# Kernel tuning notes

Measured on AMD Instinct MI355X. Metric: run time of the kernel, lower is better.

Reference implementation:

```python
import jax, jax.numpy as jnp
import numpy as np

B, C, T, H, W = 32, 384, 16, 14, 14
K, NUM_SAMPLES, SIGMA = 8, 1000, 0.05
C2 = 2 * C  # ScoreNet doubles embed_dim internally


def setup_inputs() -> dict:
    key = jax.random.key(0)
    ks = jax.random.split(key, 12)
    def rn(k, shape, s=0.02):
        return jax.random.normal(k, shape, dtype=jnp.float32) * s
    return {
        "frames": jax.random.normal(ks[0], (B, C, T, H, W), dtype=jnp.float32),
        "noise": jax.random.normal(ks[1], (B, NUM_SAMPLES, T), dtype=jnp.float32),
        "conv_w": rn(ks[2], (C, C, 1, 3, 3)),
        "conv_b": jnp.zeros((C,), jnp.float32),
        "bn_g": jnp.ones((C,), jnp.float32),
        "bn_b": jnp.zeros((C,), jnp.float32),
        "ln_g": jnp.ones((C2,), jnp.float32),
        "ln_b": jnp.zeros((C2,), jnp.float32),
        "lin_w": rn(ks[3], (C2, C2)),
        "lin_b": jnp.zeros((C2,), jnp.float32),
        "w1": rn(ks[4], (C2, C)), "b1": jnp.zeros((C,), jnp.float32),
        "w2": rn(ks[5], (C, C // 2)), "b2": jnp.zeros((C // 2,), jnp.float32),
        "w3": rn(ks[6], (C // 2, 1)), "b3": jnp.zeros((1,), jnp.float32),
    }


def score_net(frames, conv_w, conv_b, bn_g, bn_b, ln_g, ln_b, lin_w, lin_b,
              w1, b1, w2, b2, w3, b3):
    x = jax.lax.stop_gradient(frames)  # ScoreNet detaches its input
    x = jax.lax.conv_general_dilated(
        x, conv_w, window_strides=(1, 2, 2), padding='VALID',
        dimension_numbers=('NCDHW', 'OIDHW', 'NCDHW'))
    x = x + conv_b[None, :, None, None, None]
    # BatchNorm3d in training mode: biased batch stats over (N,T,H,W)
    m = x.mean(axis=(0, 2, 3, 4))
    v = x.var(axis=(0, 2, 3, 4))
    x = (x - m[None, :, None, None, None]) / jnp.sqrt(v + 1e-5)[None, :, None, None, None]
    x = x * bn_g[None, :, None, None, None] + bn_b[None, :, None, None, None]
    # b c t h w -> b t (h w) c
    b, c, t, h, w = x.shape
    x = jnp.transpose(x, (0, 2, 3, 4, 1)).reshape(b, t, h * w, c)
    x = jnp.concatenate([x.mean(axis=2), x.max(axis=2)], axis=-1)  # [B,T,2C]
    # LayerNorm(2C)
    mu = x.mean(-1, keepdims=True)
    var = x.var(-1, keepdims=True)
    x = (x - mu) / jnp.sqrt(var + 1e-5) * ln_g + ln_b
    x = jax.nn.gelu(x @ lin_w + lin_b, approximate=False)
    local_x = x[..., :C2 // 2]
    global_x = jnp.broadcast_to(x[..., C2 // 2:].mean(axis=1, keepdims=True), (b, t, C2 // 2))
    x = jnp.concatenate([local_x, global_x], axis=-1)
    x = jax.nn.gelu(x @ w1 + b1, approximate=False)
    x = jax.nn.gelu(x @ w2 + b2, approximate=False)
    score = (x @ w3 + b3)[..., 0]  # [B,T]
    smin = score.min(axis=-1, keepdims=True)
    smax = score.max(axis=-1, keepdims=True)
    return (score - smin) / (smax - smin + 1e-5)


def perturbed_indicators(score, noise):
    d = score.shape[-1]
    pert = score[:, None, :] + noise * SIGMA  # [B,N,T]
    idx_top = jnp.sort(jax.lax.top_k(pert, K)[1], axis=-1)        # [B,N,K]
    idx_back = jnp.sort(jax.lax.top_k(-pert, d - K)[1], axis=-1)  # [B,N,T-K]
    ind_top = jax.nn.one_hot(idx_top, d, dtype=jnp.float32).mean(axis=1)   # [B,K,T]
    ind_back = jax.nn.one_hot(idx_back, d, dtype=jnp.float32).mean(axis=1)  # [B,T-K,T]
    return ind_top, ind_back


def reference(frames, noise, conv_w, conv_b, bn_g, bn_b, ln_g, ln_b, lin_w, lin_b,
              w1, b1, w2, b2, w3, b3):
    score = score_net(frames, conv_w, conv_b, bn_g, bn_b, ln_g, ln_b, lin_w, lin_b,
                      w1, b1, w2, b2, w3, b3)  # [B,T]
    ind_top, ind_back = perturbed_indicators(score, noise)
    # b c t h w -> b t (h w c)
    flat = jnp.transpose(frames, (0, 2, 3, 4, 1)).reshape(B, T, H * W * C)
    p_top = jnp.einsum('bkd,bdc->bkc', ind_top, flat)
    p_back = jnp.einsum('bkd,bdc->bkc', ind_back, flat)
    frames_topk = jnp.transpose(p_top.reshape(B, K, H, W, C), (0, 4, 1, 2, 3))
    frames_back = jnp.transpose(p_back.reshape(B, T - K, H, W, C), (0, 4, 1, 2, 3))
    sorted_inds = jnp.argsort(score, axis=1)
    return frames_topk, frames_back, sorted_inds
```

## Files before the change

### kernel.cpp

```cpp
#include <hip/hip_runtime.h>
#include <hip/hip_bf16.h>
#include <cstdint>

#define NB 32
#define NC 384
#define NT 16
#define NH 14
#define NW 14
#define HWI 196
#define HOW 6
#define HWO 36
#define C2 768
#define MCONV (NB*NT*HWO)
#define KCONV 3456
#define TOPK 8
#define NSAMP 1000
#define OUT_TOPK_ELEMS (NB*NC*TOPK*HWI)
#define OUT_INDS_OFF   (2*OUT_TOPK_ELEMS)

#define OFF_FHI  0ull
#define OFF_FLO  77070336ull
#define OFF_WHI  154140672ull
#define OFF_WLO  156794880ull
#define OFF_CONV 159449088ull
#define OFF_PART 0ull
#define OFF_BNSC 221184ull
#define OFF_BNSH 222720ull
#define OFF_Y    224256ull
#define OFF_X1   1797120ull
#define OFF_GM   3369984ull
#define OFF_H1   4992000ull
#define OFF_H2   5778432ull
#define OFF_IND  6171648ull

typedef __attribute__((ext_vector_type(4))) float f32x4;
typedef __attribute__((ext_vector_type(8))) short bf16x8;

__device__ __forceinline__ unsigned short f2bf(float f) {
  unsigned u = __float_as_uint(f);
  unsigned r = (u + 0x7FFFu + ((u >> 16) & 1u)) >> 16;
  return (unsigned short)r;
}
__device__ __forceinline__ float bf2f(unsigned short u) {
  return __uint_as_float(((unsigned)u) << 16);
}

__device__ __forceinline__ void gload_lds16(const void* gptr, void* lptr) {
  __builtin_amdgcn_global_load_lds(
      (const __attribute__((address_space(1))) unsigned int*)gptr,
      (__attribute__((address_space(3))) unsigned int*)lptr, 16, 0, 0);
}

__global__ __launch_bounds__(256)
void split_frames(const float* __restrict__ fr,
                  unsigned short* __restrict__ fhi,
                  unsigned short* __restrict__ flo) {
  __shared__ unsigned int tile[64][197];
  int bid = blockIdx.x;
  int cb = bid % 6, bt = bid / 6;
  int b = bt >> 4, t = bt & 15;
  const float* src = fr + (((size_t)b * NC + cb * 64) * NT + t) * HWI;
  for (int i = threadIdx.x; i < 64 * 49; i += 256) {
    int c = i / 49, q = i - c * 49;
    float4 v = *(const float4*)(src + (size_t)c * (NT * HWI) + q * 4);
    float vv[4] = {v.x, v.y, v.z, v.w};
#pragma unroll
    for (int u = 0; u < 4; ++u) {
      unsigned short h = f2bf(vv[u]);
      unsigned short l = f2bf(vv[u] - bf2f(h));
      tile[c][q * 4 + u] = ((unsigned)h << 16) | (unsigned)l;
    }
  }
  __syncthreads();
  size_t obase = ((size_t)bt * HWI) * NC + cb * 64;
  for (int i = threadIdx.x; i < 196 * 8; i += 256) {
    int hw = i >> 3, c8 = i & 7;
    bf16x8 vh, vl;
#pragma unroll
    for (int u = 0; u < 8; ++u) {
      unsigned p = tile[c8 * 8 + u][hw];
      vh[u] = (short)(p >> 16);
      vl[u] = (short)(p & 0xffff);
    }
    size_t o = obase + (size_t)hw * NC + c8 * 8;
    *(bf16x8*)(fhi + o) = vh;
    *(bf16x8*)(flo + o) = vl;
  }
}

__global__ __launch_bounds__(256)
void split_w(const float* __restrict__ cw,
             unsigned short* __restrict__ whi,
             unsigned short* __restrict__ wlo) {
  int idx = blockIdx.x * 256 + threadIdx.x;
  int co = idx / KCONV;
  int rem = idx - co * KCONV;
  int c9 = rem / NC, ci = rem - c9 * NC;
  float v = cw[((size_t)co * NC + ci) * 9 + c9];
  unsigned short h = f2bf(v);
  unsigned short l = f2bf(v - bf2f(h));
  whi[idx] = h; wlo[idx] = l;
}

__global__ __launch_bounds__(256, 2)
void conv_gemm(const unsigned short* __restrict__ fhi,
               const unsigned short* __restrict__ flo,
               const unsigned short* __restrict__ whi,
               const unsigned short* __restrict__ wlo,
               const float* __restrict__ conv_b,
               float* __restrict__ p0,
               float* __restrict__ p1) {
  __shared__ unsigned short sAhi[128 * 32], sAlo[128 * 32];
  __shared__ unsigned short sBhi[128 * 32], sBlo[128 * 32];
  const int tid = threadIdx.x;
  const int lane = tid & 63;
  const int wv = tid >> 6;
  const int bid = blockIdx.x;
  const int bm = bid % 144;
  const int r  = bid / 144;
  const int bn = r % 3;
  const int kz = r / 3;

  int aoff[2], boff[2];
#pragma unroll
  for (int j = 0; j < 2; ++j) {
    int l = (wv * 2 + j) * 64 + lane;
    int row = l >> 2, chunk = l & 3;
    int m = bm * 128 + row;
    int wo = m % 6; int tmp = m / 6;
    int ho = tmp % 6; tmp /= 6;
    aoff[j] = ((tmp * HWI) + (2 * ho) * NW + 2 * wo) * NC + chunk * 8;
    int co = bn * 128 + row;
    boff[j] = co * KCONV + chunk * 8;
  }

  f32x4 acc[4][4];
#pragma unroll
  for (int i = 0; i < 4; ++i)
#pragma unroll
    for (int j = 0; j < 4; ++j) acc[i][j] = (f32x4){0.f, 0.f, 0.f, 0.f};

  const int wrow = (wv >> 1) * 64;
  const int wcol = (wv & 1) * 64;
  const int fr_row = lane & 15;
  const int fr_k = (lane >> 4) * 8;

  int c9 = kz ? 4 : 0;
  int rem = kz ? 6 : 0;
  for (int s = 0; s < 54; ++s) {
    int kh = c9 / 3, kw = c9 - kh * 3;
    int soffA = (kh * NW + kw) * NC + rem * 32;
    int soffB = c9 * NC + rem * 32;
#pragma unroll
    for (int j = 0; j < 2; ++j) {
      char* ldsA  = (char*)sAhi + (wv * 2 + j) * 1024;
      char* ldsAl = (char*)sAlo + (wv * 2 + j) * 1024;
      char* ldsB  = (char*)sBhi + (wv * 2 + j) * 1024;
      char* ldsBl = (char*)sBlo + (wv * 2 + j) * 1024;
      gload_lds16(fhi + aoff[j] + soffA, ldsA);
      gload_lds16(flo + aoff[j] + soffA, ldsAl);
      gload_lds16(whi + boff[j] + soffB, ldsB);
      gload_lds16(wlo + boff[j] + soffB, ldsBl);
    }
    __syncthreads();
    bf16x8 ah[4], al[4], bh[4], bl[4];
#pragma unroll
    for (int m = 0; m < 4; ++m) {
      int rr = wrow + m * 16 + fr_row;
      ah[m] = *(const bf16x8*)&sAhi[rr * 32 + fr_k];
      al[m] = *(const bf16x8*)&sAlo[rr * 32 + fr_k];
    }
#pragma unroll
    for (int n = 0; n < 4; ++n) {
      int rr = wcol + n * 16 + fr_row;
      bh[n] = *(const bf16x8*)&sBhi[rr * 32 + fr_k];
      bl[n] = *(const bf16x8*)&sBlo[rr * 32 + fr_k];
    }
#pragma unroll
    for (int m = 0; m < 4; ++m)
#pragma unroll
      for (int n = 0; n < 4; ++n) {
        acc[m][n] = __builtin_amdgcn_mfma_f32_16x16x32_bf16(ah[m], bh[n], acc[m][n], 0, 0, 0);
        acc[m][n] = __builtin_amdgcn_mfma_f32_16x16x32_bf16(ah[m], bl[n], acc[m][n], 0, 0, 0);
        acc[m][n] = __builtin_amdgcn_mfma_f32_16x16x32_bf16(al[m], bh[n], acc[m][n], 0, 0, 0);
      }
    __syncthreads();
    if (++rem == 12) { rem = 0; ++c9; }
  }

  float* dst = kz ? p1 : p0;
#pragma unroll
  for (int m = 0; m < 4; ++m)
#pragma unroll
    for (int n = 0; n < 4; ++n) {
      int col = bn * 128 + wcol + n * 16 + (lane & 15);
      float cb = kz ? 0.f : conv_b[col];
#pragma unroll
      for (int j = 0; j < 4; ++j) {
        int row = bm * 128 + wrow + m * 16 + (lane >> 4) * 4 + j;
        dst[(size_t)row * NC + col] = acc[m][n][j] + cb;
      }
    }
}

__global__ __launch_bounds__(384)
void bn_part(const float* __restrict__ p0, const float* __restrict__ p1,
             float* __restrict__ part) {
  int c = threadIdx.x;
  int r0 = blockIdx.x * 256;
  float s = 0.f, sq = 0.f;
  for (int r = 0; r < 256; ++r) {
    size_t off = (size_t)(r0 + r) * NC + c;
    float v = p0[off] + p1[off];
    s += v; sq += v * v;
  }
  part[blockIdx.x * 768 + c] = s;
  part[blockIdx.x * 768 + 384 + c] = sq;
}

__global__ __launch_bounds__(384)
void bn_fin(const float* __restrict__ part, const float* __restrict__ bn_g,
            const float* __restrict__ bn_b, float* __restrict__ bnsc,
            float* __restrict__ bnsh) {
  int c = threadIdx.x;
  float s = 0.f, sq = 0.f;
  for (int i = 0; i < 72; ++i) {
    s += part[i * 768 + c];
    sq += part[i * 768 + 384 + c];
  }
  float mean = s / (float)MCONV;
  float var = sq / (float)MCONV - mean * mean;
  float sc = bn_g[c] / sqrtf(var + 1e-5f);
  bnsc[c] = sc;
  bnsh[c] = bn_b[c] - mean * sc;
}

__global__ __launch_bounds__(384)
void pool_ln(const float* __restrict__ p0, const float* __restrict__ p1,
             const float* __restrict__ bnsc,
             const float* __restrict__ bnsh, const float* __restrict__ ln_g,
             const float* __restrict__ ln_b, float* __restrict__ y) {
  __shared__ float r1[384], r2[384], stats[2];
  int bt = blockIdx.x, c = threadIdx.x;
  float sc = bnsc[c], sh = bnsh[c];
  size_t base = (size_t)bt * HWO * NC + c;
  float sum = 0.f, mx = -1e30f;
  for (int hw = 0; hw < HWO; ++hw) {
    size_t off = base + (size_t)hw * NC;
    float v = (p0[off] + p1[off]) * sc + sh;
    sum += v;
    mx = fmaxf(mx, v);
  }
  float meanv = sum * (1.f / 36.f);
  r1[c] = meanv + mx;
  r2[c] = meanv * meanv + mx * mx;
  __syncthreads();
  for (int s = 192; s >= 6; s >>= 1) {
    if (c < s) { r1[c] += r1[c + s]; r2[c] += r2[c + s]; }
    __syncthreads();
  }
  if (c == 0) {
    float S1 = 0.f, S2 = 0.f;
    for (int i = 0; i < 6; ++i) { S1 += r1[i]; S2 += r2[i]; }
    float mu = S1 / (float)C2;
    float var = S2 / (float)C2 - mu * mu;
    stats[0] = mu;
    stats[1] = 1.0f / sqrtf(var + 1e-5f);
  }
  __syncthreads();
  float mu = stats[0], rstd = stats[1];
  y[(size_t)bt * C2 + c] = (meanv - mu) * rstd * ln_g[c] + ln_b[c];
  y[(size_t)bt * C2 + 384 + c] = (mx - mu) * rstd * ln_g[384 + c] + ln_b[384 + c];
}

template <int GELU, int X2>
__global__ __launch_bounds__(256)
void gemm64(const float* __restrict__ A, const float* __restrict__ gmv,
            const float* __restrict__ Wm,
            const float* __restrict__ bias, float* __restrict__ Cm,
            int K, int N) {
  __shared__ float As[64][17];
  __shared__ float Bs[16][68];
  int tid = threadIdx.x;
  int tx = tid & 15, ty = tid >> 4;
  int m0 = blockIdx.y * 64, n0 = blockIdx.x * 64;
  int ar = tid >> 2, ak = (tid & 3) * 4;
  int br = tid >> 4, bc = (tid & 15) * 4;
  float acc[4][4] = {};
  for (int kt = 0; kt < K; kt += 16) {
    int kcol = kt + ak;
    float4 av;
    if (X2 && kcol >= 384)
      av = *(const float4*)(gmv + ((m0 + ar) >> 4) * 384 + (kcol - 384));
    else
      av = *(const float4*)(A + (size_t)(m0 + ar) * K + kcol);
    float4 bv = *(const float4*)(Wm + (size_t)(kt + br) * N + n0 + bc);
    As[ar][ak + 0] = av.x; As[ar][ak + 1] = av.y;
    As[ar][ak + 2] = av.z; As[ar][ak + 3] = av.w;
    Bs[br][bc + 0] = bv.x; Bs[br][bc + 1] = bv.y;
    Bs[br][bc + 2] = bv.z; Bs[br][bc + 3] = bv.w;
    __syncthreads();
#pragma unroll
    for (int kk = 0; kk < 16; ++kk) {
      float a0 = As[ty * 4 + 0][kk], a1 = As[ty * 4 + 1][kk];
      float a2 = As[ty * 4 + 2][kk], a3 = As[ty * 4 + 3][kk];
      float b0 = Bs[kk][tx * 4 + 0], b1 = Bs[kk][tx * 4 + 1];
      float b2 = Bs[kk][tx * 4 + 2], b3 = Bs[kk][tx * 4 + 3];
      acc[0][0] += a0 * b0; acc[0][1] += a0 * b1; acc[0][2] += a0 * b2; acc[0][3] += a0 * b3;
      acc[1][0] += a1 * b0; acc[1][1] += a1 * b1; acc[1][2] += a1 * b2; acc[1][3] += a1 * b3;
      acc[2][0] += a2 * b0; acc[2][1] += a2 * b1; acc[2][2] += a2 * b2; acc[2][3] += a2 * b3;
      acc[3][0] += a3 * b0; acc[3][1] += a3 * b1; acc[3][2] += a3 * b2; acc[3][3] += a3 * b3;
    }
    __syncthreads();
  }
#pragma unroll
  for (int i = 0; i < 4; ++i) {
    int row = m0 + ty * 4 + i;
#pragma unroll
    for (int j = 0; j < 4; ++j) {
      int col = n0 + tx * 4 + j;
      float v = acc[i][j] + bias[col];
      if (GELU) v = 0.5f * v * (1.0f + erff(v * 0.70710678118654752f));
      Cm[(size_t)row * N + col] = v;
    }
  }
}

__global__ __launch_bounds__(384)
void gmean_k(const float* __restrict__ x1, float* __restrict__ gm) {
  int b = blockIdx.x, c = threadIdx.x;
  float s = 0.f;
  for (int t = 0; t < NT; ++t) s += x1[((size_t)b * NT + t) * C2 + 384 + c];
  gm[b * 384 + c] = s * (1.f / 16.f);
}

__global__ __launch_bounds__(256)
void score_head(const float* __restrict__ h2, const float* __restrict__ w3,
                const float* __restrict__ b3, const float* __restrict__ noise,
                float* __restrict__ ind, float* __restrict__ out_inds) {
  int b = blockIdx.x;
  int tid = threadIdx.x;
  int lane = tid & 63, wv = tid >> 6;
  __shared__ float sv[16], sn[16];
  __shared__ unsigned cnt[256];
  for (int t = wv; t < 16; t += 4) {
    const float* hr = h2 + ((size_t)b * 16 + t) * 192;
    float p = 0.f;
    for (int i = lane; i < 192; i += 64) p += hr[i] * w3[i];
#pragma unroll
    for (int off = 32; off; off >>= 1) p += __shfl_down(p, off, 64);
    if (lane == 0) sv[t] = p + b3[0];
  }
  cnt[tid] = 0;
  __syncthreads();
  if (tid == 0) {
    float mn = sv[0], mx = sv[0];
    for (int t = 1; t < 16; ++t) { mn = fminf(mn, sv[t]); mx = fmaxf(mx, sv[t]); }
    float inv = 1.0f / (mx - mn + 1e-5f);
    for (int t = 0; t < 16; ++t) sn[t] = (sv[t] - mn) * inv;
  }
  __syncthreads();
  if (tid < 16) {
    int t = tid, r = 0;
    for (int u = 0; u < 16; ++u)
      r += (sv[u] < sv[t]) || (sv[u] == sv[t] && u < t);
    out_inds[b * 16 + r] = (float)t;
  }
  for (int s = tid; s < NSAMP; s += 256) {
    const float* nz = noise + ((size_t)b * NSAMP + s) * 16;
    float pert[16];
#pragma unroll
    for (int t = 0; t < 16; ++t) pert[t] = sn[t] + 0.05f * nz[t];
    unsigned tm = 0, bm2 = 0;
#pragma unroll
    for (int t = 0; t < 16; ++t) {
      int ct = 0, cb = 0;
#pragma unroll
      for (int u = 0; u < 16; ++u) {
        ct += (pert[u] > pert[t]) || (pert[u] == pert[t] && u < t);
        cb += (pert[u] < pert[t]) || (pert[u] == pert[t] && u < t);
      }
      if (ct < 8) tm |= 1u << t;
      if (cb < 8) bm2 |= 1u << t;
    }
    int j = 0, jb = 0;
#pragma unroll
    for (int t = 0; t < 16; ++t) {
      if (tm & (1u << t)) { if (j < 8) atomicAdd(&cnt[j * 16 + t], 1u); ++j; }
      if (bm2 & (1u << t)) { if (jb < 8) atomicAdd(&cnt[128 + jb * 16 + t], 1u); ++jb; }
    }
  }
  __syncthreads();
  ind[b * 256 + tid] = (float)cnt[tid] / 1000.0f;
}

__global__ __launch_bounds__(256)
void gather_k(const float* __restrict__ frames, const float* __restrict__ ind,
              float* __restrict__ out) {
  int bc = blockIdx.x;
  int b = bc / NC;
  __shared__ float wt[256];
  wt[threadIdx.x] = ind[b * 256 + threadIdx.x];
  __syncthreads();
  int hw = threadIdx.x;
  if (hw >= HWI) return;
  const float* src = frames + (size_t)bc * NT * HWI + hw;
  float v[16];
#pragma unroll
  for (int t = 0; t < 16; ++t) v[t] = src[t * HWI];
  size_t obase = (size_t)bc * TOPK * HWI + hw;
#pragma unroll
  for (int k = 0; k < TOPK; ++k) {
    float st = 0.f, sb = 0.f;
#pragma unroll
    for (int t = 0; t < 16; ++t) {
      st += wt[k * 16 + t] * v[t];
      sb += wt[128 + k * 16 + t] * v[t];
    }
    out[obase + k * HWI] = st;
    out[OUT_TOPK_ELEMS + obase + k * HWI] = sb;
  }
}

extern "C" void kernel_launch(void* const* d_in, const int* in_sizes, int n_in,
                              void* d_out, int out_size, void* d_ws, size_t ws_size,
                              hipStream_t stream) {
  const float* frames = (const float*)d_in[0];
  const float* noise  = (const float*)d_in[1];
  const float* conv_w = (const float*)d_in[2];
  const float* conv_b = (const float*)d_in[3];
  const float* bn_g   = (const float*)d_in[4];
  const float* bn_b   = (const float*)d_in[5];
  const float* ln_g   = (const float*)d_in[6];
  const float* ln_b   = (const float*)d_in[7];
  const float* lin_w  = (const float*)d_in[8];
  const float* lin_b  = (const float*)d_in[9];
  const float* w1     = (const float*)d_in[10];
  const float* b1     = (const float*)d_in[11];
  const float* w2     = (const float*)d_in[12];
  const float* b2     = (const float*)d_in[13];
  const float* w3     = (const float*)d_in[14];
  const float* b3     = (const float*)d_in[15];

  char* ws = (char*)d_ws;
  unsigned short* fhi = (unsigned short*)(ws + OFF_FHI);
  unsigned short* flo = (unsigned short*)(ws + OFF_FLO);
  unsigned short* whi = (unsigned short*)(ws + OFF_WHI);
  unsigned short* wlo = (unsigned short*)(ws + OFF_WLO);
  float* p0    = (float*)(ws + OFF_CONV);
  float* part  = (float*)(ws + OFF_PART);
  float* bnsc  = (float*)(ws + OFF_BNSC);
  float* bnsh  = (float*)(ws + OFF_BNSH);
  float* y     = (float*)(ws + OFF_Y);
  float* x1    = (float*)(ws + OFF_X1);
  float* gm    = (float*)(ws + OFF_GM);
  float* h1    = (float*)(ws + OFF_H1);
  float* h2    = (float*)(ws + OFF_H2);
  float* ind   = (float*)(ws + OFF_IND);
  float* out   = (float*)d_out;
  float* p1    = out;

  split_frames<<<3072, 256, 0, stream>>>(frames, fhi, flo);
  split_w<<<5184, 256, 0, stream>>>(conv_w, whi, wlo);
  conv_gemm<<<864, 256, 0, stream>>>(fhi, flo, whi, wlo, conv_b, p0, p1);
  bn_part<<<72, 384, 0, stream>>>(p0, p1, part);
  bn_fin<<<1, 384, 0, stream>>>(part, bn_g, bn_b, bnsc, bnsh);
  pool_ln<<<512, 384, 0, stream>>>(p0, p1, bnsc, bnsh, ln_g, ln_b, y);
  gemm64<1, 0><<<dim3(12, 8), 256, 0, stream>>>(y, nullptr, lin_w, lin_b, x1, 768, 768);
  gmean_k<<<32, 384, 0, stream>>>(x1, gm);
  gemm64<1, 1><<<dim3(6, 8), 256, 0, stream>>>(x1, gm, w1, b1, h1, 768, 384);
  gemm64<1, 0><<<dim3(3, 8), 256, 0, stream>>>(h1, nullptr, w2, b2, h2, 384, 192);
  score_head<<<32, 256, 0, stream>>>(h2, w3, b3, noise, ind, out + OUT_INDS_OFF);
  gather_k<<<12288, 256, 0, stream>>>(frames, ind, out);
}
```

Baseline: 520.7 us.

## Swizzle conv LDS, stage weight split, parallelize score head and vectorize gather

Several independent changes land together. The conv GEMM gets an XOR swizzle on LDS chunk placement to reduce bank conflicts and a higher occupancy launch bound. split_w now stages each output channel in shared memory so its global reads are coalesced. bn_part gets twice as many blocks, score_head splits the noise samples over 8 blocks per batch and writes partial counts that gather_k sums, and gather_k handles 4 channels per block with float4 loads and stores. The risks are register pressure from the occupancy hint and redundant partial-count reduction in every gather block.

```diff
diff --git a/kernel.cpp b/kernel.cpp
--- a/kernel.cpp
+++ b/kernel.cpp
@@ -24,14 +24,14 @@
 #define OFF_WLO  156794880ull
 #define OFF_CONV 159449088ull
 #define OFF_PART 0ull
-#define OFF_BNSC 221184ull
-#define OFF_BNSH 222720ull
-#define OFF_Y    224256ull
-#define OFF_X1   1797120ull
-#define OFF_GM   3369984ull
-#define OFF_H1   4992000ull
-#define OFF_H2   5778432ull
-#define OFF_IND  6171648ull
+#define OFF_BNSC 442368ull
+#define OFF_BNSH 443904ull
+#define OFF_Y    445440ull
+#define OFF_X1   2018304ull
+#define OFF_GM   3591168ull
+#define OFF_H1   3640320ull
+#define OFF_H2   4426752ull
+#define OFF_IND  4819968ull
 
 typedef __attribute__((ext_vector_type(4))) float f32x4;
 typedef __attribute__((ext_vector_type(8))) short bf16x8;
@@ -92,17 +92,23 @@
 void split_w(const float* __restrict__ cw,
              unsigned short* __restrict__ whi,
              unsigned short* __restrict__ wlo) {
-  int idx = blockIdx.x * 256 + threadIdx.x;
-  int co = idx / KCONV;
-  int rem = idx - co * KCONV;
-  int c9 = rem / NC, ci = rem - c9 * NC;
-  float v = cw[((size_t)co * NC + ci) * 9 + c9];
-  unsigned short h = f2bf(v);
-  unsigned short l = f2bf(v - bf2f(h));
-  whi[idx] = h; wlo[idx] = l;
-}
-
-__global__ __launch_bounds__(256, 2)
+  __shared__ float t[KCONV];
+  int co = blockIdx.x;
+  const float* src = cw + (size_t)co * KCONV;
+  for (int i = threadIdx.x; i < KCONV / 4; i += 256)
+    *(float4*)&t[i * 4] = *(const float4*)&src[i * 4];
+  __syncthreads();
+  unsigned short* oh = whi + (size_t)co * KCONV;
+  unsigned short* ol = wlo + (size_t)co * KCONV;
+  for (int i = threadIdx.x; i < KCONV; i += 256) {
+    int c9 = i / NC, ci = i - c9 * NC;
+    float v = t[ci * 9 + c9];
+    unsigned short h = f2bf(v);
+    oh[i] = h; ol[i] = f2bf(v - bf2f(h));
+  }
+}
+
+__global__ __launch_bounds__(256, 4)
 void conv_gemm(const unsigned short* __restrict__ fhi,
                const unsigned short* __restrict__ flo,
                const unsigned short* __restrict__ whi,
@@ -125,7 +131,8 @@
 #pragma unroll
   for (int j = 0; j < 2; ++j) {
     int l = (wv * 2 + j) * 64 + lane;
-    int row = l >> 2, chunk = l & 3;
+    int row = l >> 2;
+    int chunk = (l & 3) ^ ((l >> 3) & 3);
     int m = bm * 128 + row;
     int wo = m % 6; int tmp = m / 6;
     int ho = tmp % 6; tmp /= 6;
@@ -143,7 +150,7 @@
   const int wrow = (wv >> 1) * 64;
   const int wcol = (wv & 1) * 64;
   const int fr_row = lane & 15;
-  const int fr_k = (lane >> 4) * 8;
+  const int slot8 = (((lane >> 4) ^ ((fr_row >> 1) & 3))) * 8;
 
   int c9 = kz ? 4 : 0;
   int rem = kz ? 6 : 0;
@@ -167,14 +174,14 @@
 #pragma unroll
     for (int m = 0; m < 4; ++m) {
       int rr = wrow + m * 16 + fr_row;
-      ah[m] = *(const bf16x8*)&sAhi[rr * 32 + fr_k];
-      al[m] = *(const bf16x8*)&sAlo[rr * 32 + fr_k];
+      ah[m] = *(const bf16x8*)&sAhi[rr * 32 + slot8];
+      al[m] = *(const bf16x8*)&sAlo[rr * 32 + slot8];
     }
 #pragma unroll
     for (int n = 0; n < 4; ++n) {
       int rr = wcol + n * 16 + fr_row;
-      bh[n] = *(const bf16x8*)&sBhi[rr * 32 + fr_k];
-      bl[n] = *(const bf16x8*)&sBlo[rr * 32 + fr_k];
+      bh[n] = *(const bf16x8*)&sBhi[rr * 32 + slot8];
+      bl[n] = *(const bf16x8*)&sBlo[rr * 32 + slot8];
     }
 #pragma unroll
     for (int m = 0; m < 4; ++m)
@@ -207,9 +214,9 @@
 void bn_part(const float* __restrict__ p0, const float* __restrict__ p1,
              float* __restrict__ part) {
   int c = threadIdx.x;
-  int r0 = blockIdx.x * 256;
+  int r0 = blockIdx.x * 128;
   float s = 0.f, sq = 0.f;
-  for (int r = 0; r < 256; ++r) {
+  for (int r = 0; r < 128; ++r) {
     size_t off = (size_t)(r0 + r) * NC + c;
     float v = p0[off] + p1[off];
     s += v; sq += v * v;
@@ -224,7 +231,7 @@
             float* __restrict__ bnsh) {
   int c = threadIdx.x;
   float s = 0.f, sq = 0.f;
-  for (int i = 0; i < 72; ++i) {
+  for (int i = 0; i < 144; ++i) {
     s += part[i * 768 + c];
     sq += part[i * 768 + 384 + c];
   }
@@ -337,8 +344,8 @@
 __global__ __launch_bounds__(256)
 void score_head(const float* __restrict__ h2, const float* __restrict__ w3,
                 const float* __restrict__ b3, const float* __restrict__ noise,
-                float* __restrict__ ind, float* __restrict__ out_inds) {
-  int b = blockIdx.x;
+                unsigned* __restrict__ pcnt, float* __restrict__ out_inds) {
+  int b = blockIdx.x >> 3, chunk = blockIdx.x & 7;
   int tid = threadIdx.x;
   int lane = tid & 63, wv = tid >> 6;
   __shared__ float sv[16], sn[16];
@@ -360,13 +367,14 @@
     for (int t = 0; t < 16; ++t) sn[t] = (sv[t] - mn) * inv;
   }
   __syncthreads();
-  if (tid < 16) {
+  if (chunk == 0 && tid < 16) {
     int t = tid, r = 0;
     for (int u = 0; u < 16; ++u)
       r += (sv[u] < sv[t]) || (sv[u] == sv[t] && u < t);
     out_inds[b * 16 + r] = (float)t;
   }
-  for (int s = tid; s < NSAMP; s += 256) {
+  if (tid < 125) {
+    int s = chunk * 125 + tid;
     const float* nz = noise + ((size_t)b * NSAMP + s) * 16;
     float pert[16];
 #pragma unroll
@@ -391,34 +399,44 @@
     }
   }
   __syncthreads();
-  ind[b * 256 + tid] = (float)cnt[tid] / 1000.0f;
+  pcnt[(size_t)(b * 8 + chunk) * 256 + tid] = cnt[tid];
 }
 
 __global__ __launch_bounds__(256)
-void gather_k(const float* __restrict__ frames, const float* __restrict__ ind,
+void gather_k(const float* __restrict__ frames, const unsigned* __restrict__ pcnt,
               float* __restrict__ out) {
-  int bc = blockIdx.x;
-  int b = bc / NC;
+  int bid = blockIdx.x;
+  int tid = threadIdx.x;
+  int b = (bid * 4) / NC;
   __shared__ float wt[256];
-  wt[threadIdx.x] = ind[b * 256 + threadIdx.x];
-  __syncthreads();
-  int hw = threadIdx.x;
-  if (hw >= HWI) return;
-  const float* src = frames + (size_t)bc * NT * HWI + hw;
-  float v[16];
-#pragma unroll
-  for (int t = 0; t < 16; ++t) v[t] = src[t * HWI];
-  size_t obase = (size_t)bc * TOPK * HWI + hw;
+  {
+    unsigned s = 0;
+    const unsigned* pc = pcnt + (size_t)b * 8 * 256 + tid;
+#pragma unroll
+    for (int ch = 0; ch < 8; ++ch) s += pc[ch * 256];
+    wt[tid] = (float)s / 1000.0f;
+  }
+  __syncthreads();
+  if (tid >= 196) return;
+  int cc = tid / 49, q = tid - cc * 49;
+  int bc = bid * 4 + cc;
+  const float4* src = (const float4*)(frames + (size_t)bc * NT * HWI) + q;
+  float4 v[16];
+#pragma unroll
+  for (int t = 0; t < 16; ++t) v[t] = src[t * 49];
+  float4* o1 = (float4*)(out + (size_t)bc * TOPK * HWI) + q;
+  float4* o2 = (float4*)(out + OUT_TOPK_ELEMS + (size_t)bc * TOPK * HWI) + q;
 #pragma unroll
   for (int k = 0; k < TOPK; ++k) {
-    float st = 0.f, sb = 0.f;
+    float4 st = {0.f, 0.f, 0.f, 0.f}, sb = {0.f, 0.f, 0.f, 0.f};
 #pragma unroll
     for (int t = 0; t < 16; ++t) {
-      st += wt[k * 16 + t] * v[t];
-      sb += wt[128 + k * 16 + t] * v[t];
-    }
-    out[obase + k * HWI] = st;
-    out[OUT_TOPK_ELEMS + obase + k * HWI] = sb;
+      float a = wt[k * 16 + t], bw = wt[128 + k * 16 + t];
+      st.x += a * v[t].x; st.y += a * v[t].y; st.z += a * v[t].z; st.w += a * v[t].w;
+      sb.x += bw * v[t].x; sb.y += bw * v[t].y; sb.z += bw * v[t].z; sb.w += bw * v[t].w;
+    }
+    o1[k * 49] = st;
+    o2[k * 49] = sb;
   }
 }
 
@@ -456,20 +474,20 @@
   float* gm    = (float*)(ws + OFF_GM);
   float* h1    = (float*)(ws + OFF_H1);
   float* h2    = (float*)(ws + OFF_H2);
-  float* ind   = (float*)(ws + OFF_IND);
+  unsigned* pcnt = (unsigned*)(ws + OFF_IND);
   float* out   = (float*)d_out;
   float* p1    = out;
 
   split_frames<<<3072, 256, 0, stream>>>(frames, fhi, flo);
-  split_w<<<5184, 256, 0, stream>>>(conv_w, whi, wlo);
+  split_w<<<384, 256, 0, stream>>>(conv_w, whi, wlo);
   conv_gemm<<<864, 256, 0, stream>>>(fhi, flo, whi, wlo, conv_b, p0, p1);
-  bn_part<<<72, 384, 0, stream>>>(p0, p1, part);
+  bn_part<<<144, 384, 0, stream>>>(p0, p1, part);
   bn_fin<<<1, 384, 0, stream>>>(part, bn_g, bn_b, bnsc, bnsh);
   pool_ln<<<512, 384, 0, stream>>>(p0, p1, bnsc, bnsh, ln_g, ln_b, y);
   gemm64<1, 0><<<dim3(12, 8), 256, 0, stream>>>(y, nullptr, lin_w, lin_b, x1, 768, 768);
   gmean_k<<<32, 384, 0, stream>>>(x1, gm);
   gemm64<1, 1><<<dim3(6, 8), 256, 0, stream>>>(x1, gm, w1, b1, h1, 768, 384);
   gemm64<1, 0><<<dim3(3, 8), 256, 0, stream>>>(h1, nullptr, w2, b2, h2, 384, 192);
-  score_head<<<32, 256, 0, stream>>>(h2, w3, b3, noise, ind, out + OUT_INDS_OFF);
-  gather_k<<<12288, 256, 0, stream>>>(frames, ind, out);
-}
+  score_head<<<256, 256, 0, stream>>>(h2, w3, b3, noise, pcnt, out + OUT_INDS_OFF);
+  gather_k<<<3072, 256, 0, stream>>>(frames, pcnt, out);
+}
```

Result: faster. 497.4 us (-4.5%).
